# Kernel optimization log

Measured on AMD Instinct MI355X. Metric: run time of the kernel, lower is better.

Reference implementation:

```python
import jax, jax.numpy as jnp
import numpy as np

D_MODEL = 2048
NUM_EXPERTS = 128
TOP_K = 8
NORM_P = 2.0  # normalize_expert_weights


def setup_inputs() -> dict:
    key = jax.random.key(0)
    k1, k2 = jax.random.split(key)
    x = jax.random.normal(k1, (4, 4096, D_MODEL), dtype=jnp.float32)
    # router weight ~ trunc_normal(std=0.02); plain normal*0.02 is fine for a numeric baseline
    weight = jax.random.normal(k2, (NUM_EXPERTS, D_MODEL), dtype=jnp.float32) * 0.02
    score_bias = jnp.zeros((NUM_EXPERTS,), dtype=jnp.float32)
    return {"x": x, "weight": weight, "score_bias": score_bias}


def reference(x, weight, score_bias):
    # Flatten tokens: (B, S, D) -> (N, D); router always runs in fp32 (x.float())
    B, S, D = x.shape
    xf = x.reshape(B * S, D).astype(jnp.float32)
    # get_expert_logits: F.linear(x, weight.view(E, D)) -> (N, E)
    logits = jnp.einsum("nd,ed->ne", xf, weight.astype(jnp.float32))
    # softmax gating
    scores = jax.nn.softmax(logits, axis=-1)
    # bias-adjusted top-k (bias only affects selection, not the returned weights)
    biased = scores + score_bias[None, :]
    _, expert_indices = jax.lax.top_k(biased, TOP_K)          # (N, top_k)
    expert_weights = jnp.take_along_axis(scores, expert_indices, axis=-1)
    # normalize_expert_weights = 2.0 -> divide by L2 norm across top_k
    norm = jnp.linalg.norm(expert_weights, ord=NORM_P, axis=-1, keepdims=True)
    expert_weights = expert_weights / norm
    return expert_weights, expert_indices
```

## Files before the change

### kernel.cpp

```cpp
#include <hip/hip_runtime.h>
#include <math.h>


#define NE     128
#define TOKT   128
#define KC     32
#define KS     4
#define DMODEL 2048
#define DSLICE (DMODEL / KS)
#define CHUNK_SH (3 * NE * KC)

typedef __attribute__((ext_vector_type(8))) short short8;
typedef __attribute__((ext_vector_type(4))) short s16x4;
typedef __attribute__((ext_vector_type(4))) float f32x4;

union S8  { short s[8]; short8 v; };
union S4u { short s[4]; s16x4 v; };

__device__ __forceinline__ void split3(float f, S8& hi, S8& mi, S8& lo, int j) {
  const unsigned u0 = __float_as_uint(f);
  const float hif = __uint_as_float(u0 & 0xFFFF0000u);
  const float r1 = f - hif;
  const unsigned u1 = __float_as_uint(r1);
  const float mif = __uint_as_float(u1 & 0xFFFF0000u);
  const float r2 = r1 - mif;
  hi.s[j] = (short)(u0 >> 16);
  mi.s[j] = (short)(u1 >> 16);
  lo.s[j] = (short)(__float_as_uint(r2) >> 16);
}

__device__ __forceinline__ void split3w(float f, S4u& hi, S4u& mi, S4u& lo, int j) {
  const unsigned u0 = __float_as_uint(f);
  const float hif = __uint_as_float(u0 & 0xFFFF0000u);
  const float r1 = f - hif;
  const unsigned u1 = __float_as_uint(r1);
  const float mif = __uint_as_float(u1 & 0xFFFF0000u);
  const float r2 = r1 - mif;
  hi.s[j] = (short)(u0 >> 16);
  mi.s[j] = (short)(u1 >> 16);
  lo.s[j] = (short)(__float_as_uint(r2) >> 16);
}

__global__ __launch_bounds__(256) void wprep(const float* __restrict__ w,
                                             short* __restrict__ wp) {
  const int gid = blockIdx.x * 256 + threadIdx.x;
  const int e = gid >> 9;
  const int g = gid & 511;
  const int k = g << 2;
  const int chunk = k >> 5;
  const int kk = k & 31;
  const f32x4 a = *(const f32x4*)(w + (size_t)e * DMODEL + k);
  S4u hi, mi, lo;
  split3w(a[0], hi, mi, lo, 0); split3w(a[1], hi, mi, lo, 1);
  split3w(a[2], hi, mi, lo, 2); split3w(a[3], hi, mi, lo, 3);
  short* base = wp + (size_t)chunk * CHUNK_SH + (size_t)e * KC + kk;
  *(s16x4*)(base)               = hi.v;
  *(s16x4*)(base + NE * KC)     = mi.v;
  *(s16x4*)(base + 2 * NE * KC) = lo.v;
}

__device__ __forceinline__ void gll16(const short* g, short* l) {
  __builtin_amdgcn_global_load_lds(
      (const __attribute__((address_space(1))) void*)g,
      (__attribute__((address_space(3))) void*)l, 16, 0, 0);
}

__global__ __launch_bounds__(256) void logits_mfma(
    const float* __restrict__ x, const short* __restrict__ wp,
    float* __restrict__ part, int N) {
  __shared__ short xs[3][TOKT][KC];
  __shared__ __align__(16) short wsm[3][NE][KC];

  const int tid  = threadIdx.x;
  const int wave = tid >> 6;
  const int lane = tid & 63;
  const int wm = wave >> 1;
  const int wn = wave & 1;
  const int quad = lane >> 4;
  const int l16  = lane & 15;
  const size_t tokBase = (size_t)blockIdx.x * TOKT;
  const int d0 = blockIdx.y * DSLICE;

  const int r = tid >> 1;
  const int h = tid & 1;

  f32x4 acc[4][4];
#pragma unroll
  for (int i = 0; i < 4; ++i)
#pragma unroll
    for (int j = 0; j < 4; ++j) acc[i][j] = (f32x4)(0.f);

  for (int kc = 0; kc < DSLICE; kc += KC) {
    __syncthreads();
    {
      const float* gx = x + (tokBase + r) * DMODEL + d0 + kc + h * 16;
#pragma unroll
      for (int run = 0; run < 2; ++run) {
        const float4 a0 = *(const float4*)(gx + run * 8);
        const float4 a1 = *(const float4*)(gx + run * 8 + 4);
        S8 hi, mi, lo;
        split3(a0.x, hi, mi, lo, 0); split3(a0.y, hi, mi, lo, 1);
        split3(a0.z, hi, mi, lo, 2); split3(a0.w, hi, mi, lo, 3);
        split3(a1.x, hi, mi, lo, 4); split3(a1.y, hi, mi, lo, 5);
        split3(a1.z, hi, mi, lo, 6); split3(a1.w, hi, mi, lo, 7);
        const int kk = h * 16 + run * 8;
        *(short8*)&xs[0][r][kk] = hi.v;
        *(short8*)&xs[1][r][kk] = mi.v;
        *(short8*)&xs[2][r][kk] = lo.v;
      }
    }
    {
      const int chunk = blockIdx.y * (DSLICE / KC) + (kc >> 5);
      const short* gsrc = wp + (size_t)chunk * CHUNK_SH + wave * 512 + lane * 8;
      short* ldst = &wsm[0][0][0] + wave * 512;
#pragma unroll
      for (int issue = 0; issue < 6; ++issue)
        gll16(gsrc + issue * 2048, ldst + issue * 2048);
    }
    __syncthreads();

    short8 af[4][3];
#pragma unroll
    for (int mt = 0; mt < 4; ++mt)
#pragma unroll
      for (int p = 0; p < 3; ++p)
        af[mt][p] = *(const short8*)&xs[p][wm * 64 + mt * 16 + l16][quad * 8];

#pragma unroll
    for (int nt = 0; nt < 4; ++nt) {
      short8 bf[3];
#pragma unroll
      for (int p = 0; p < 3; ++p)
        bf[p] = *(const short8*)&wsm[p][wn * 64 + nt * 16 + l16][quad * 8];
#pragma unroll
      for (int mt = 0; mt < 4; ++mt) {
        f32x4 c = acc[mt][nt];
        c = __builtin_amdgcn_mfma_f32_16x16x32_bf16(af[mt][0], bf[0], c, 0, 0, 0);
        c = __builtin_amdgcn_mfma_f32_16x16x32_bf16(af[mt][0], bf[1], c, 0, 0, 0);
        c = __builtin_amdgcn_mfma_f32_16x16x32_bf16(af[mt][1], bf[0], c, 0, 0, 0);
        c = __builtin_amdgcn_mfma_f32_16x16x32_bf16(af[mt][0], bf[2], c, 0, 0, 0);
        c = __builtin_amdgcn_mfma_f32_16x16x32_bf16(af[mt][2], bf[0], c, 0, 0, 0);
        c = __builtin_amdgcn_mfma_f32_16x16x32_bf16(af[mt][1], bf[1], c, 0, 0, 0);
        acc[mt][nt] = c;
      }
    }
  }

#pragma unroll
  for (int mt = 0; mt < 4; ++mt)
#pragma unroll
    for (int nt = 0; nt < 4; ++nt) {
      const int ex = wn * 64 + nt * 16 + l16;
#pragma unroll
      for (int reg = 0; reg < 4; ++reg) {
        const size_t tok = tokBase + wm * 64 + mt * 16 + quad * 4 + reg;
        part[((size_t)blockIdx.y * N + tok) * NE + ex] = acc[mt][nt][reg];
      }
    }
}

__global__ __launch_bounds__(256) void router_topk(
    const float* __restrict__ part, const float* __restrict__ bias,
    float* __restrict__ outW, float* __restrict__ outI, int ks, int N) {
  const int wave = threadIdx.x >> 6;
  const int lane = threadIdx.x & 63;
  const int token = blockIdx.x * 4 + wave;
  if (token >= N) return;

  float l0 = 0.f, l1 = 0.f;
  for (int k = 0; k < ks; ++k) {
    const float* p = part + ((size_t)k * N + token) * NE;
    l0 += p[lane];
    l1 += p[lane + 64];
  }

  float m = fmaxf(l0, l1);
#pragma unroll
  for (int off = 1; off < 64; off <<= 1) m = fmaxf(m, __shfl_xor(m, off));
  const float ev0 = __expf(l0 - m);
  const float ev1 = __expf(l1 - m);
  float zs = ev0 + ev1;
#pragma unroll
  for (int off = 1; off < 64; off <<= 1) zs += __shfl_xor(zs, off);
  const float s0 = ev0 / zs;
  const float s1 = ev1 / zs;

  float b0 = s0 + bias[lane];
  float b1 = s1 + bias[lane + 64];

  float myv = 0.f;
  int myi = 0;
  float ss = 0.f;
#pragma unroll
  for (int rnd = 0; rnd < 8; ++rnd) {
    float key; int idx;
    if (b0 >= b1) { key = b0; idx = lane; }
    else          { key = b1; idx = lane + 64; }
#pragma unroll
    for (int off = 1; off < 64; off <<= 1) {
      const float k2 = __shfl_xor(key, off);
      const int   i2 = __shfl_xor(idx, off);
      if (k2 > key || (k2 == key && i2 < idx)) { key = k2; idx = i2; }
    }
    const float cand = (idx < 64) ? s0 : s1;
    const float sw = __shfl(cand, idx & 63);
    ss = fmaf(sw, sw, ss);
    if (lane == rnd) { myv = sw; myi = idx; }
    if (lane == (idx & 63)) { if (idx < 64) b0 = -INFINITY; else b1 = -INFINITY; }
  }

  const float inv = 1.f / sqrtf(ss);
  if (lane < 8) {
    outW[(size_t)token * 8 + lane] = myv * inv;
    outI[(size_t)token * 8 + lane] = (float)myi;
  }
}

extern "C" void kernel_launch(void* const* d_in, const int* in_sizes, int n_in,
                              void* d_out, int out_size, void* d_ws, size_t ws_size,
                              hipStream_t stream) {
  const float* x    = (const float*)d_in[0];
  const float* w    = (const float*)d_in[1];
  const float* bias = (const float*)d_in[2];
  float* out = (float*)d_out;

  const int N = in_sizes[0] / DMODEL;
  short* wp  = (short*)d_ws;
  float* part = (float*)((char*)d_ws + (4 << 20));

  wprep<<<256, 256, 0, stream>>>(w, wp);
  logits_mfma<<<dim3(N / TOKT, KS), 256, 0, stream>>>(x, wp, part, N);
  router_topk<<<(N + 3) / 4, 256, 0, stream>>>(part, bias, out, out + (size_t)N * 8, KS, N);
}
```

Baseline: 231.2 us.

## Software-pipeline logits GEMM with double-buffered weight LDS and register-prefetched x

Restructures the main K loop of the router logits MFMA kernel into a two-stage software pipeline. The weight tiles are double-buffered in LDS via global_load_lds, and x chunks are prefetched into registers two iterations ahead. Explicit vmcnt waits and barriers replace the per-iteration full syncs. The aim is to overlap global memory latency with MFMA compute, at the cost of more registers and LDS, and of fragile hand-counted waitcnt values.

Measured after the change: 231.1 us. About the same (-0.0%).

```diff
diff --git a/kernel.cpp b/kernel.cpp
--- a/kernel.cpp
+++ b/kernel.cpp
@@ -8,6 +8,7 @@
 #define KS     4
 #define DMODEL 2048
 #define DSLICE (DMODEL / KS)
+#define NCH    (DSLICE / KC)
 #define CHUNK_SH (3 * NE * KC)
 
 typedef __attribute__((ext_vector_type(8))) short short8;
@@ -69,7 +70,7 @@
     const float* __restrict__ x, const short* __restrict__ wp,
     float* __restrict__ part, int N) {
   __shared__ short xs[3][TOKT][KC];
-  __shared__ __align__(16) short wsm[3][NE][KC];
+  __shared__ __align__(16) short wsm[2][3][NE][KC];
 
   const int tid  = threadIdx.x;
   const int wave = tid >> 6;
@@ -80,9 +81,11 @@
   const int l16  = lane & 15;
   const size_t tokBase = (size_t)blockIdx.x * TOKT;
   const int d0 = blockIdx.y * DSLICE;
+  const int chunkBase = blockIdx.y * NCH;
 
   const int r = tid >> 1;
   const int h = tid & 1;
+  const float* gx = x + (tokBase + r) * DMODEL + d0 + h * 16;
 
   f32x4 acc[4][4];
 #pragma unroll
@@ -90,48 +93,49 @@
 #pragma unroll
     for (int j = 0; j < 4; ++j) acc[i][j] = (f32x4)(0.f);
 
-  for (int kc = 0; kc < DSLICE; kc += KC) {
-    __syncthreads();
-    {
-      const float* gx = x + (tokBase + r) * DMODEL + d0 + kc + h * 16;
-#pragma unroll
-      for (int run = 0; run < 2; ++run) {
-        const float4 a0 = *(const float4*)(gx + run * 8);
-        const float4 a1 = *(const float4*)(gx + run * 8 + 4);
-        S8 hi, mi, lo;
-        split3(a0.x, hi, mi, lo, 0); split3(a0.y, hi, mi, lo, 1);
-        split3(a0.z, hi, mi, lo, 2); split3(a0.w, hi, mi, lo, 3);
-        split3(a1.x, hi, mi, lo, 4); split3(a1.y, hi, mi, lo, 5);
-        split3(a1.z, hi, mi, lo, 6); split3(a1.w, hi, mi, lo, 7);
-        const int kk = h * 16 + run * 8;
-        *(short8*)&xs[0][r][kk] = hi.v;
-        *(short8*)&xs[1][r][kk] = mi.v;
-        *(short8*)&xs[2][r][kk] = lo.v;
-      }
-    }
-    {
-      const int chunk = blockIdx.y * (DSLICE / KC) + (kc >> 5);
-      const short* gsrc = wp + (size_t)chunk * CHUNK_SH + wave * 512 + lane * 8;
-      short* ldst = &wsm[0][0][0] + wave * 512;
-#pragma unroll
-      for (int issue = 0; issue < 6; ++issue)
-        gll16(gsrc + issue * 2048, ldst + issue * 2048);
-    }
-    __syncthreads();
-
+  auto stage_w = [&](int buf, int c) {
+    const short* gsrc = wp + (size_t)(chunkBase + c) * CHUNK_SH + wave * 512 + lane * 8;
+    short* ldst = &wsm[buf][0][0][0] + wave * 512;
+#pragma unroll
+    for (int i = 0; i < 6; ++i)
+      gll16(gsrc + i * 2048, ldst + i * 2048);
+  };
+  auto load_x = [&](float4 (&xr)[4], int t) {
+    const float* g = gx + t * KC;
+    xr[0] = *(const float4*)(g);
+    xr[1] = *(const float4*)(g + 4);
+    xr[2] = *(const float4*)(g + 8);
+    xr[3] = *(const float4*)(g + 12);
+  };
+  auto stage_x = [&](const float4 (&xr)[4]) {
+#pragma unroll
+    for (int run = 0; run < 2; ++run) {
+      const float4 a0 = xr[2 * run];
+      const float4 a1 = xr[2 * run + 1];
+      S8 hi, mi, lo;
+      split3(a0.x, hi, mi, lo, 0); split3(a0.y, hi, mi, lo, 1);
+      split3(a0.z, hi, mi, lo, 2); split3(a0.w, hi, mi, lo, 3);
+      split3(a1.x, hi, mi, lo, 4); split3(a1.y, hi, mi, lo, 5);
+      split3(a1.z, hi, mi, lo, 6); split3(a1.w, hi, mi, lo, 7);
+      const int kk = h * 16 + run * 8;
+      *(short8*)&xs[0][r][kk] = hi.v;
+      *(short8*)&xs[1][r][kk] = mi.v;
+      *(short8*)&xs[2][r][kk] = lo.v;
+    }
+  };
+  auto compute = [&](int buf) {
     short8 af[4][3];
 #pragma unroll
     for (int mt = 0; mt < 4; ++mt)
 #pragma unroll
       for (int p = 0; p < 3; ++p)
         af[mt][p] = *(const short8*)&xs[p][wm * 64 + mt * 16 + l16][quad * 8];
-
 #pragma unroll
     for (int nt = 0; nt < 4; ++nt) {
       short8 bf[3];
 #pragma unroll
       for (int p = 0; p < 3; ++p)
-        bf[p] = *(const short8*)&wsm[p][wn * 64 + nt * 16 + l16][quad * 8];
+        bf[p] = *(const short8*)&wsm[buf][p][wn * 64 + nt * 16 + l16][quad * 8];
 #pragma unroll
       for (int mt = 0; mt < 4; ++mt) {
         f32x4 c = acc[mt][nt];
@@ -144,7 +148,47 @@
         acc[mt][nt] = c;
       }
     }
-  }
+  };
+
+  float4 xA[4], xB[4];
+  stage_w(0, 0);
+  load_x(xA, 0);
+  load_x(xB, 1);
+
+#pragma unroll 1
+  for (int t = 0; t < NCH - 2; t += 2) {
+    stage_x(xA);
+    stage_w(1, t + 1);
+    load_x(xA, t + 2);
+    asm volatile("s_waitcnt vmcnt(10) lgkmcnt(0)" ::: "memory");
+    __builtin_amdgcn_s_barrier();
+    __builtin_amdgcn_sched_barrier(0);
+    compute(0);
+    __builtin_amdgcn_s_barrier();
+    __builtin_amdgcn_sched_barrier(0);
+    stage_x(xB);
+    stage_w(0, t + 2);
+    load_x(xB, t + 3);
+    asm volatile("s_waitcnt vmcnt(10) lgkmcnt(0)" ::: "memory");
+    __builtin_amdgcn_s_barrier();
+    __builtin_amdgcn_sched_barrier(0);
+    compute(1);
+    __builtin_amdgcn_s_barrier();
+    __builtin_amdgcn_sched_barrier(0);
+  }
+  stage_x(xA);
+  stage_w(1, NCH - 1);
+  asm volatile("s_waitcnt vmcnt(6) lgkmcnt(0)" ::: "memory");
+  __builtin_amdgcn_s_barrier();
+  __builtin_amdgcn_sched_barrier(0);
+  compute(0);
+  __builtin_amdgcn_s_barrier();
+  __builtin_amdgcn_sched_barrier(0);
+  stage_x(xB);
+  asm volatile("s_waitcnt vmcnt(0) lgkmcnt(0)" ::: "memory");
+  __builtin_amdgcn_s_barrier();
+  __builtin_amdgcn_sched_barrier(0);
+  compute(1);
 
 #pragma unroll
   for (int mt = 0; mt < 4; ++mt)
```

## Load x directly into MFMA fragments and software-pipeline x loads with weight staging

Applied to the files above, without the earlier changes.

Removes the shared-memory staging of x: each lane loads its own fp32 slice of x straight into registers and splits it into bf16 hi/mid/lo fragments. The next chunk's x is prefetched into a second register set while the current chunk is computed, with explicit vmcnt waits and barriers around weight staging. The token tile drops from 128 to 64 and launch bounds ask for 4 blocks per CU to raise occupancy. In exchange, each weight chunk is reused by fewer tokens, so more weight traffic goes through LDS, and the hand-tuned waitcnt counts depend on the order in which the compiler issues loads.

New measurement: 247.7 us. +7.2%, slower.

```diff
diff --git a/kernel.cpp b/kernel.cpp
--- a/kernel.cpp
+++ b/kernel.cpp
@@ -3,11 +3,12 @@
 
 
 #define NE     128
-#define TOKT   128
+#define TOKT   64
 #define KC     32
 #define KS     4
 #define DMODEL 2048
 #define DSLICE (DMODEL / KS)
+#define NCH    (DSLICE / KC)
 #define CHUNK_SH (3 * NE * KC)
 
 typedef __attribute__((ext_vector_type(8))) short short8;
@@ -65,10 +66,9 @@
       (__attribute__((address_space(3))) void*)l, 16, 0, 0);
 }
 
-__global__ __launch_bounds__(256) void logits_mfma(
+__global__ __launch_bounds__(256, 4) void logits_mfma(
     const float* __restrict__ x, const short* __restrict__ wp,
     float* __restrict__ part, int N) {
-  __shared__ short xs[3][TOKT][KC];
   __shared__ __align__(16) short wsm[3][NE][KC];
 
   const int tid  = threadIdx.x;
@@ -80,52 +80,46 @@
   const int l16  = lane & 15;
   const size_t tokBase = (size_t)blockIdx.x * TOKT;
   const int d0 = blockIdx.y * DSLICE;
-
-  const int r = tid >> 1;
-  const int h = tid & 1;
-
-  f32x4 acc[4][4];
-#pragma unroll
-  for (int i = 0; i < 4; ++i)
+  const int chunkBase = blockIdx.y * NCH;
+
+  const float* xg0 = x + (tokBase + wm * 32 + l16) * (size_t)DMODEL + d0 + quad * 8;
+  const float* xg1 = xg0 + 16 * (size_t)DMODEL;
+
+  f32x4 acc[2][4];
+#pragma unroll
+  for (int i = 0; i < 2; ++i)
 #pragma unroll
     for (int j = 0; j < 4; ++j) acc[i][j] = (f32x4)(0.f);
 
-  for (int kc = 0; kc < DSLICE; kc += KC) {
-    __syncthreads();
-    {
-      const float* gx = x + (tokBase + r) * DMODEL + d0 + kc + h * 16;
-#pragma unroll
-      for (int run = 0; run < 2; ++run) {
-        const float4 a0 = *(const float4*)(gx + run * 8);
-        const float4 a1 = *(const float4*)(gx + run * 8 + 4);
-        S8 hi, mi, lo;
-        split3(a0.x, hi, mi, lo, 0); split3(a0.y, hi, mi, lo, 1);
-        split3(a0.z, hi, mi, lo, 2); split3(a0.w, hi, mi, lo, 3);
-        split3(a1.x, hi, mi, lo, 4); split3(a1.y, hi, mi, lo, 5);
-        split3(a1.z, hi, mi, lo, 6); split3(a1.w, hi, mi, lo, 7);
-        const int kk = h * 16 + run * 8;
-        *(short8*)&xs[0][r][kk] = hi.v;
-        *(short8*)&xs[1][r][kk] = mi.v;
-        *(short8*)&xs[2][r][kk] = lo.v;
-      }
-    }
-    {
-      const int chunk = blockIdx.y * (DSLICE / KC) + (kc >> 5);
-      const short* gsrc = wp + (size_t)chunk * CHUNK_SH + wave * 512 + lane * 8;
-      short* ldst = &wsm[0][0][0] + wave * 512;
-#pragma unroll
-      for (int issue = 0; issue < 6; ++issue)
-        gll16(gsrc + issue * 2048, ldst + issue * 2048);
-    }
-    __syncthreads();
-
-    short8 af[4][3];
-#pragma unroll
-    for (int mt = 0; mt < 4; ++mt)
-#pragma unroll
-      for (int p = 0; p < 3; ++p)
-        af[mt][p] = *(const short8*)&xs[p][wm * 64 + mt * 16 + l16][quad * 8];
-
+  auto stage_w = [&](int c) {
+    const short* gsrc = wp + (size_t)(chunkBase + c) * CHUNK_SH + wave * 512 + lane * 8;
+    short* ldst = &wsm[0][0][0] + wave * 512;
+#pragma unroll
+    for (int i = 0; i < 6; ++i)
+      gll16(gsrc + i * 2048, ldst + i * 2048);
+  };
+  auto load_x = [&](float4 (&xr)[4], int t) {
+    const float* g0 = xg0 + t * KC;
+    const float* g1 = xg1 + t * KC;
+    xr[0] = *(const float4*)(g0);
+    xr[1] = *(const float4*)(g0 + 4);
+    xr[2] = *(const float4*)(g1);
+    xr[3] = *(const float4*)(g1 + 4);
+  };
+  auto build_af = [&](short8 (&af)[2][3], const float4 (&xr)[4]) {
+#pragma unroll
+    for (int mt = 0; mt < 2; ++mt) {
+      const float4 a0 = xr[2 * mt];
+      const float4 a1 = xr[2 * mt + 1];
+      S8 hi, mi, lo;
+      split3(a0.x, hi, mi, lo, 0); split3(a0.y, hi, mi, lo, 1);
+      split3(a0.z, hi, mi, lo, 2); split3(a0.w, hi, mi, lo, 3);
+      split3(a1.x, hi, mi, lo, 4); split3(a1.y, hi, mi, lo, 5);
+      split3(a1.z, hi, mi, lo, 6); split3(a1.w, hi, mi, lo, 7);
+      af[mt][0] = hi.v; af[mt][1] = mi.v; af[mt][2] = lo.v;
+    }
+  };
+  auto compute = [&](const short8 (&af)[2][3]) {
 #pragma unroll
     for (int nt = 0; nt < 4; ++nt) {
       short8 bf[3];
@@ -133,7 +127,7 @@
       for (int p = 0; p < 3; ++p)
         bf[p] = *(const short8*)&wsm[p][wn * 64 + nt * 16 + l16][quad * 8];
 #pragma unroll
-      for (int mt = 0; mt < 4; ++mt) {
+      for (int mt = 0; mt < 2; ++mt) {
         f32x4 c = acc[mt][nt];
         c = __builtin_amdgcn_mfma_f32_16x16x32_bf16(af[mt][0], bf[0], c, 0, 0, 0);
         c = __builtin_amdgcn_mfma_f32_16x16x32_bf16(af[mt][0], bf[1], c, 0, 0, 0);
@@ -144,16 +138,53 @@
         acc[mt][nt] = c;
       }
     }
-  }
-
-#pragma unroll
-  for (int mt = 0; mt < 4; ++mt)
+  };
+
+  float4 xa[4], xb[4];
+  load_x(xa, 0);
+  stage_w(0);
+
+  short8 af[2][3];
+#pragma unroll 1
+  for (int t = 0; t < NCH; t += 2) {
+    build_af(af, xa);
+    if (t + 1 < NCH) load_x(xb, t + 1);
+    if (t + 1 < NCH)
+      asm volatile("s_waitcnt vmcnt(4)" ::: "memory");
+    else
+      asm volatile("s_waitcnt vmcnt(0)" ::: "memory");
+    __builtin_amdgcn_s_barrier();
+    __builtin_amdgcn_sched_barrier(0);
+    compute(af);
+    if (t + 1 < NCH) {
+      __builtin_amdgcn_s_barrier();
+      __builtin_amdgcn_sched_barrier(0);
+      stage_w(t + 1);
+      build_af(af, xb);
+      if (t + 2 < NCH) load_x(xa, t + 2);
+      if (t + 2 < NCH)
+        asm volatile("s_waitcnt vmcnt(4)" ::: "memory");
+      else
+        asm volatile("s_waitcnt vmcnt(0)" ::: "memory");
+      __builtin_amdgcn_s_barrier();
+      __builtin_amdgcn_sched_barrier(0);
+      compute(af);
+      if (t + 2 < NCH) {
+        __builtin_amdgcn_s_barrier();
+        __builtin_amdgcn_sched_barrier(0);
+        stage_w(t + 2);
+      }
+    }
+  }
+
+#pragma unroll
+  for (int mt = 0; mt < 2; ++mt)
 #pragma unroll
     for (int nt = 0; nt < 4; ++nt) {
       const int ex = wn * 64 + nt * 16 + l16;
 #pragma unroll
       for (int reg = 0; reg < 4; ++reg) {
-        const size_t tok = tokBase + wm * 64 + mt * 16 + quad * 4 + reg;
+        const size_t tok = tokBase + wm * 32 + mt * 16 + quad * 4 + reg;
         part[((size_t)blockIdx.y * N + tok) * NE + ex] = acc[mt][nt][reg];
       }
     }
```
